# Optimization experiments

Hardware: AMD Instinct MI355X
Metric: run time of the kernel (lower is better)

## Reference

```python
import jax, jax.numpy as jnp
import numpy as np

B, C, H, W = 2, 512, 64, 64
G = 32  # GroupNorm groups
EPS = 1e-6


def setup_inputs() -> dict:
    key = jax.random.key(0)
    ks = jax.random.split(key, 6)
    s = 1.0 / np.sqrt(C)
    return {
        "x": jax.random.normal(ks[0], (B, C, H, W), dtype=jnp.float32),
        "gn_w": jnp.ones((C,), dtype=jnp.float32),
        "gn_b": jnp.zeros((C,), dtype=jnp.float32),
        "wq": jax.random.normal(ks[1], (C, C), dtype=jnp.float32) * s,
        "bq": jnp.zeros((C,), dtype=jnp.float32),
        "wk": jax.random.normal(ks[2], (C, C), dtype=jnp.float32) * s,
        "bk": jnp.zeros((C,), dtype=jnp.float32),
        "wv": jax.random.normal(ks[3], (C, C), dtype=jnp.float32) * s,
        "bv": jnp.zeros((C,), dtype=jnp.float32),
        "wo": jax.random.normal(ks[4], (C, C), dtype=jnp.float32) * s,
        "bo": jnp.zeros((C,), dtype=jnp.float32),
    }


def _group_norm(x, w, b):
    b_, c_, h_, w_ = x.shape
    xg = x.reshape(b_, G, c_ // G, h_ * w_)
    mu = jnp.mean(xg, axis=(2, 3), keepdims=True)
    var = jnp.var(xg, axis=(2, 3), keepdims=True)
    xn = (xg - mu) * jax.lax.rsqrt(var + EPS)
    xn = xn.reshape(b_, c_, h_ * w_)
    return xn * w[None, :, None] + b[None, :, None]  # [B, C, N]


def reference(x, gn_w, gn_b, wq, bq, wk, bk, wv, bv, wo, bo):
    b, c, h, w = x.shape
    hn = _group_norm(x, gn_w, gn_b)  # [B, C, N]
    # 1x1 convs == per-pixel matmuls over channel dim
    q = jnp.einsum('oc,bcn->bon', wq, hn) + bq[None, :, None]
    k = jnp.einsum('oc,bcn->bon', wk, hn) + bk[None, :, None]
    v = jnp.einsum('oc,bcn->bon', wv, hn) + bv[None, :, None]
    scale = jnp.asarray(c, x.dtype) ** -0.5
    attn = jnp.einsum('bci,bcj->bij', q, k) * scale  # [B, N, N]
    attn = jax.nn.softmax(attn, axis=-1)
    o = jnp.einsum('bij,bcj->bci', attn, v)  # [B, C, N]
    o = jnp.einsum('oc,bcn->bon', wo, o) + bo[None, :, None]
    return x + o.reshape(b, c, h, w)
```

## Files before the change

kernel.cpp:

```cpp
#include <hip/hip_runtime.h>

#define CC 512
#define NPIX 4096
#define NB 2
#define NG 32
#define GSIZE 16
#define EPS 1e-6f

typedef unsigned short u16;
typedef __bf16 bf16x8 __attribute__((ext_vector_type(8)));
typedef float f32x4 __attribute__((ext_vector_type(4)));

__device__ __forceinline__ float bf2f(u16 u) {
  union { unsigned int i; float f; } c; c.i = ((unsigned int)u) << 16; return c.f;
}
__device__ __forceinline__ u16 f2bf(float f) {
  union { float f; unsigned int i; } c; c.f = f;
  unsigned int u = c.i;
  return (u16)((u + 0x7fffu + ((u >> 16) & 1u)) >> 16);
}

__global__ __launch_bounds__(256) void f2bf4x4_kernel(
    const float* __restrict__ s0, const float* __restrict__ s1,
    const float* __restrict__ s2, const float* __restrict__ s3,
    u16* __restrict__ d0, u16* __restrict__ d1,
    u16* __restrict__ d2, u16* __restrict__ d3) {
  const float* s; u16* d;
  switch (blockIdx.y) {
    case 0: s = s0; d = d0; break;
    case 1: s = s1; d = d1; break;
    case 2: s = s2; d = d2; break;
    default: s = s3; d = d3; break;
  }
  int i = blockIdx.x * 256 + threadIdx.x;
  float4 v = ((const float4*)s)[i];
  uint2 pk;
  pk.x = (unsigned)f2bf(v.x) | ((unsigned)f2bf(v.y) << 16);
  pk.y = (unsigned)f2bf(v.z) | ((unsigned)f2bf(v.w) << 16);
  ((uint2*)d)[i] = pk;
}

__global__ __launch_bounds__(256) void concat2_kernel(const float* __restrict__ a,
                                                      const float* __restrict__ b,
                                                      float* __restrict__ o) {
  int i = blockIdx.x * 256 + threadIdx.x;
  o[i] = (i < CC) ? a[i] : b[i - CC];
}

__global__ __launch_bounds__(256) void gn_stats_kernel(const float* __restrict__ x,
                                                       float* __restrict__ stats) {
  int bg = blockIdx.x;
  const float4* p = (const float4*)(x + (long)bg * (GSIZE * NPIX));
  float s = 0.f, ss = 0.f;
  for (int i = threadIdx.x; i < GSIZE * NPIX / 4; i += 256) {
    float4 v = p[i];
    s  += v.x + v.y + v.z + v.w;
    ss += v.x * v.x + v.y * v.y + v.z * v.z + v.w * v.w;
  }
  for (int off = 32; off; off >>= 1) { s += __shfl_xor(s, off); ss += __shfl_xor(ss, off); }
  __shared__ float rs[4], rss[4];
  int wid = threadIdx.x >> 6;
  if ((threadIdx.x & 63) == 0) { rs[wid] = s; rss[wid] = ss; }
  __syncthreads();
  if (threadIdx.x == 0) {
    s = rs[0] + rs[1] + rs[2] + rs[3];
    ss = rss[0] + rss[1] + rss[2] + rss[3];
    float mean = s / (float)(GSIZE * NPIX);
    float var = ss / (float)(GSIZE * NPIX) - mean * mean;
    stats[bg * 2] = mean;
    stats[bg * 2 + 1] = rsqrtf(var + EPS);
  }
}

__global__ __launch_bounds__(256) void gn_apply_kernel(const float* __restrict__ x,
                                                       const float* __restrict__ stats,
                                                       const float* __restrict__ gw,
                                                       const float* __restrict__ gb,
                                                       u16* __restrict__ hn) {
  int n0 = blockIdx.x * 64, c0 = blockIdx.y * 64, b = blockIdx.z;
  __shared__ float tile[64][65];
  int t = threadIdx.x;
  int nj = t & 63, cw = t >> 6;
  #pragma unroll
  for (int r = 0; r < 16; ++r) {
    int ci = cw * 16 + r;
    int c = c0 + ci;
    float mean = stats[(b * NG + (c >> 4)) * 2];
    float rstd = stats[(b * NG + (c >> 4)) * 2 + 1];
    float v = x[((long)b * CC + c) * NPIX + n0 + nj];
    tile[ci][nj] = (v - mean) * rstd * gw[c] + gb[c];
  }
  __syncthreads();
  #pragma unroll
  for (int r = 0; r < 16; ++r) {
    int nn = cw * 16 + r;
    hn[((long)b * NPIX + n0 + nn) * CC + c0 + nj] = f2bf(tile[nj][nn]);
  }
}

#define BM 128
#define BN 128
#define BKT 64
#define BUFSZ 8192

template<int OUTF32, int BIASMODE, int RESID>
__global__ __launch_bounds__(256) void gemm_nt(
    const u16* __restrict__ A, int lda, long aBatch,
    const u16* __restrict__ B, int ldb, long bBatch,
    void* __restrict__ C, int ldc, long cBatch,
    const float* __restrict__ bias,
    const float* __restrict__ resid, long rBatch,
    int K, float scale) {
  __shared__ u16 SH[2 * 2 * BUFSZ];
  const int t = threadIdx.x;

  int nwgx = gridDim.x, nwgy = gridDim.y;
  int flat = blockIdx.x + nwgx * (blockIdx.y + nwgy * blockIdx.z);
  int nwg = nwgx * nwgy * gridDim.z;
  int newflat = (flat % 8) * (nwg / 8) + flat / 8;
  const int bx = newflat % nwgx;
  int tmpf = newflat / nwgx;
  const int by = tmpf % nwgy;
  const int bz = tmpf / nwgy;

  const int m0 = by * BM;
  const int n0 = bx * BN;
  const u16* Ab = A + (long)bz * aBatch;
  const u16* Bb = B + (long)bz * bBatch;

  const int lane = t & 63;
  const int wid = t >> 6;
  const int wr = (wid >> 1) * 64;
  const int wc = (wid & 1) * 64;
  const int r16 = lane & 15;
  const int q = lane >> 4;

  const int sRow = wid * 8 + (lane >> 3);
  const int sCol = (((lane & 7) ^ (lane >> 3)) * 8);

  f32x4 acc[4][4] = {};
  const int rsw = r16 & 7;

  const int nt = K / BKT;

  auto stage = [&](int c, int k0) {
    u16* aDst = SH + c * 2 * BUFSZ + wid * 512;
    u16* bDst = SH + c * 2 * BUFSZ + BUFSZ + wid * 512;
    #pragma unroll
    for (int p = 0; p < 4; ++p) {
      __builtin_amdgcn_global_load_lds(
          (const __attribute__((address_space(1))) unsigned int*)(Ab + (long)(m0 + p * 32 + sRow) * lda + k0 + sCol),
          (__attribute__((address_space(3))) unsigned int*)(aDst + p * 2048),
          16, 0, 0);
      __builtin_amdgcn_global_load_lds(
          (const __attribute__((address_space(1))) unsigned int*)(Bb + (long)(n0 + p * 32 + sRow) * ldb + k0 + sCol),
          (__attribute__((address_space(3))) unsigned int*)(bDst + p * 2048),
          16, 0, 0);
    }
  };

  stage(0, 0);

  for (int tt = 0; tt < nt; ++tt) {
    const int pre = tt + 1;
    if (pre < nt) {
      stage(pre & 1, pre * BKT);
      asm volatile("s_waitcnt vmcnt(8)" ::: "memory");
    } else {
      asm volatile("s_waitcnt vmcnt(0)" ::: "memory");
    }
    __builtin_amdgcn_s_barrier();
    __builtin_amdgcn_sched_barrier(0);

    const u16* As_b = SH + (tt & 1) * 2 * BUFSZ;
    const u16* Bs_b = As_b + BUFSZ;
    #pragma unroll
    for (int kk = 0; kk < BKT; kk += 32) {
      bf16x8 af[4], bfr[4];
      const int c0q = (kk >> 3) + q;
      const int colSw = (c0q ^ rsw) * 8;
      #pragma unroll
      for (int i = 0; i < 4; ++i) {
        af[i]  = *(const bf16x8*)&As_b[(wr + i * 16 + r16) * BKT + colSw];
        bfr[i] = *(const bf16x8*)&Bs_b[(wc + i * 16 + r16) * BKT + colSw];
      }
      #pragma unroll
      for (int i = 0; i < 4; ++i)
        #pragma unroll
        for (int j = 0; j < 4; ++j)
          acc[i][j] = __builtin_amdgcn_mfma_f32_16x16x32_bf16(af[i], bfr[j], acc[i][j], 0, 0, 0);
    }
    __builtin_amdgcn_s_barrier();
    __builtin_amdgcn_sched_barrier(0);
  }

  #pragma unroll
  for (int i = 0; i < 4; ++i) {
    #pragma unroll
    for (int j = 0; j < 4; ++j) {
      #pragma unroll
      for (int r = 0; r < 4; ++r) {
        int row = m0 + wr + i * 16 + q * 4 + r;
        int col = n0 + wc + j * 16 + r16;
        float v = acc[i][j][r] * scale;
        if (BIASMODE == 1) v += bias[row];
        if (BIASMODE == 2) v += bias[col];
        long off = (long)bz * cBatch + (long)row * ldc + col;
        if (RESID) v += resid[(long)bz * rBatch + (long)row * ldc + col];
        if (OUTF32) ((float*)C)[off] = v;
        else        ((u16*)C)[off] = f2bf(v);
      }
    }
  }
}

__global__ __launch_bounds__(256) void softmax_kernel(u16* __restrict__ SP, long bStride) {
  u16* p = SP + (long)blockIdx.y * bStride + (long)blockIdx.x * NPIX;
  int t = threadIdx.x;
  float v[16];
  uint4 raw0 = *(const uint4*)(p + t * 8);
  uint4 raw1 = *(const uint4*)(p + 2048 + t * 8);
  const u16* u0 = (const u16*)&raw0;
  const u16* u1 = (const u16*)&raw1;
  #pragma unroll
  for (int i = 0; i < 8; ++i) { v[i] = bf2f(u0[i]); v[8 + i] = bf2f(u1[i]); }
  float m = v[0];
  #pragma unroll
  for (int i = 1; i < 16; ++i) m = fmaxf(m, v[i]);
  for (int off = 32; off; off >>= 1) m = fmaxf(m, __shfl_xor(m, off));
  __shared__ float red[4], red2[4];
  int wid = t >> 6;
  if ((t & 63) == 0) red[wid] = m;
  __syncthreads();
  m = fmaxf(fmaxf(red[0], red[1]), fmaxf(red[2], red[3]));
  float s = 0.f;
  #pragma unroll
  for (int i = 0; i < 16; ++i) { v[i] = __expf(v[i] - m); s += v[i]; }
  for (int off = 32; off; off >>= 1) s += __shfl_xor(s, off);
  if ((t & 63) == 0) red2[wid] = s;
  __syncthreads();
  s = red2[0] + red2[1] + red2[2] + red2[3];
  float inv = 1.0f / s;
  u16 o0[8], o1[8];
  #pragma unroll
  for (int i = 0; i < 8; ++i) { o0[i] = f2bf(v[i] * inv); o1[i] = f2bf(v[8 + i] * inv); }
  *(uint4*)(p + t * 8) = *(uint4*)o0;
  *(uint4*)(p + 2048 + t * 8) = *(uint4*)o1;
}

extern "C" void kernel_launch(void* const* d_in, const int* in_sizes, int n_in,
                              void* d_out, int out_size, void* d_ws, size_t ws_size,
                              hipStream_t stream) {
  const float* x   = (const float*)d_in[0];
  const float* gnw = (const float*)d_in[1];
  const float* gnb = (const float*)d_in[2];
  const float* wq  = (const float*)d_in[3];
  const float* bq  = (const float*)d_in[4];
  const float* wk  = (const float*)d_in[5];
  const float* bk_ = (const float*)d_in[6];
  const float* wv  = (const float*)d_in[7];
  const float* bv  = (const float*)d_in[8];
  const float* wo  = (const float*)d_in[9];
  const float* bo  = (const float*)d_in[10];
  float* out = (float*)d_out;

  char* wsp = (char*)d_ws;
  auto alloc = [&](size_t bytes) {
    char* r = wsp; wsp += (bytes + 255) & ~(size_t)255; return r;
  };
  u16* wqb = (u16*)alloc((size_t)CC * CC * 2);
  u16* wkb = (u16*)alloc((size_t)CC * CC * 2);
  u16* wvb = (u16*)alloc((size_t)CC * CC * 2);
  u16* wob = (u16*)alloc((size_t)CC * CC * 2);
  float* bqk = (float*)alloc((size_t)2 * CC * 4);
  float* stats = (float*)alloc((size_t)NB * NG * 2 * 4);
  u16* hn  = (u16*)alloc((size_t)NB * NPIX * CC * 2);
  u16* qkt = (u16*)alloc((size_t)NB * NPIX * (2 * CC) * 2);
  u16* vcn = (u16*)alloc((size_t)NB * CC * NPIX * 2);
  u16* ot  = (u16*)alloc((size_t)NB * NPIX * CC * 2);
  size_t used = (size_t)(wsp - (char*)d_ws);
  size_t rem = ws_size > used ? ws_size - used : 0;
  int CH = 256;
  if ((size_t)NB * 1024 * NPIX * 2 <= rem) CH = 1024;
  if ((size_t)NB * 4096 * NPIX * 2 <= rem) CH = 4096;
  u16* SP = (u16*)alloc((size_t)NB * CH * NPIX * 2);

  dim3 blk(256);
  f2bf4x4_kernel<<<dim3(CC * CC / 1024, 4), blk, 0, stream>>>(
      wq, wk, wv, wo, wqb, wkb, wvb, wob);
  concat2_kernel<<<2 * CC / 256, blk, 0, stream>>>(bq, bk_, bqk);

  gn_stats_kernel<<<NB * NG, blk, 0, stream>>>(x, stats);
  gn_apply_kernel<<<dim3(NPIX / 64, CC / 64, NB), blk, 0, stream>>>(x, stats, gnw, gnb, hn);

  gemm_nt<0, 2, 0><<<dim3(2 * CC / BN, NPIX / BM, NB), blk, 0, stream>>>(
      hn, CC, (long)NPIX * CC, wqb, CC, 0, qkt, 2 * CC, (long)NPIX * 2 * CC,
      bqk, nullptr, 0, CC, 1.0f);
  gemm_nt<0, 1, 0><<<dim3(NPIX / BN, CC / BM, NB), blk, 0, stream>>>(
      wvb, CC, 0, hn, CC, (long)NPIX * CC, vcn, NPIX, (long)CC * NPIX, bv, nullptr, 0, CC, 1.0f);

  const u16* qt = qkt;
  const u16* kt = qkt + CC;
  const float scale = 0.044194173824159216f;
  for (int i0 = 0; i0 < NPIX; i0 += CH) {
    gemm_nt<0, 0, 0><<<dim3(NPIX / BN, CH / BM, NB), blk, 0, stream>>>(
        qt + (long)i0 * 2 * CC, 2 * CC, (long)NPIX * 2 * CC, kt, 2 * CC, (long)NPIX * 2 * CC,
        SP, NPIX, (long)CH * NPIX, nullptr, nullptr, 0, CC, scale);
    softmax_kernel<<<dim3(CH, NB), blk, 0, stream>>>(SP, (long)CH * NPIX);
    gemm_nt<0, 0, 0><<<dim3(CC / BN, CH / BM, NB), blk, 0, stream>>>(
        SP, NPIX, (long)CH * NPIX, vcn, NPIX, (long)CC * NPIX,
        ot + (long)i0 * CC, CC, (long)NPIX * CC, nullptr, nullptr, 0, NPIX, 1.0f);
  }

  gemm_nt<1, 1, 1><<<dim3(NPIX / BN, CC / BM, NB), blk, 0, stream>>>(
      wob, CC, 0, ot, CC, (long)NPIX * CC, out, NPIX, (long)CC * NPIX,
      bo, x, (long)CC * NPIX, CC, 1.0f);
}
```

Baseline: 188.9 us.

## Add 256x256-tile double-buffered MFMA GEMM for the QK^T score computation

Adds a new 512-thread GEMM kernel with 256x256 output tiles, direct global-to-LDS loads with XOR swizzling, double-buffered K staging, workgroup remapping across XCDs, and setprio around MFMA bursts. It replaces the generic tiled GEMM for the attention score matrix, but only when the whole query range is processed in one chunk (CH == 4096). The aim is more data reuse per tile and overlap of loads with MFMA compute on the largest GEMM. In exchange it uses 128 KB of LDS per block and a large accumulator register footprint, and it is inactive if CH is smaller.

```diff
diff --git a/kernel.cpp b/kernel.cpp
--- a/kernel.cpp
+++ b/kernel.cpp
@@ -212,6 +212,153 @@
       }
     }
   }
+}
+
+__global__ __launch_bounds__(512, 2) void gemm256_nt(
+    const u16* __restrict__ A, int lda, long aBatch,
+    const u16* __restrict__ B, int ldb, long bBatch,
+    u16* __restrict__ C, int ldc, long cBatch,
+    int K, float scale) {
+  __shared__ u16 SH[2][32768];
+  const int t = threadIdx.x;
+
+  int nwgx = gridDim.x, nwgy = gridDim.y;
+  int flat = blockIdx.x + nwgx * (blockIdx.y + nwgy * blockIdx.z);
+  int nwg = nwgx * nwgy * gridDim.z;
+  int newflat = (flat % 8) * (nwg / 8) + flat / 8;
+  const int bx = newflat % nwgx;
+  int tmpf = newflat / nwgx;
+  const int by = tmpf % nwgy;
+  const int bz = tmpf / nwgy;
+
+  const int m0 = by * 256;
+  const int n0 = bx * 256;
+  const u16* Ab = A + (long)bz * aBatch;
+  const u16* Bb = B + (long)bz * bBatch;
+  u16* Cb = C + (long)bz * cBatch;
+
+  const int lane = t & 63;
+  const int wid = t >> 6;
+  const int wrow = (wid >> 2) * 128;
+  const int wcol = (wid & 3) * 64;
+  const int r16 = lane & 15;
+  const int q = lane >> 4;
+  const int rsw = r16 & 7;
+
+  const int sRow = t >> 3;
+  const int sCol = ((t & 7) ^ ((t >> 3) & 7)) * 8;
+
+  auto stage = [&](int d, int k0) {
+    u16* base = &SH[d][0];
+    #pragma unroll
+    for (int i = 0; i < 4; ++i)
+      __builtin_amdgcn_global_load_lds(
+          (const __attribute__((address_space(1))) unsigned int*)(Ab + (long)(m0 + i * 64 + sRow) * lda + k0 + sCol),
+          (__attribute__((address_space(3))) unsigned int*)(base + i * 4096 + wid * 512),
+          16, 0, 0);
+    #pragma unroll
+    for (int i = 0; i < 4; ++i)
+      __builtin_amdgcn_global_load_lds(
+          (const __attribute__((address_space(1))) unsigned int*)(Bb + (long)(n0 + i * 64 + sRow) * ldb + k0 + sCol),
+          (__attribute__((address_space(3))) unsigned int*)(base + 16384 + i * 4096 + wid * 512),
+          16, 0, 0);
+  };
+
+  f32x4 acc[8][4] = {};
+  const int nt = K / 64;
+
+  stage(0, 0);
+
+  for (int tt = 0; tt < nt; ++tt) {
+    const u16* As_ = &SH[tt & 1][0];
+    const u16* Bs_ = As_ + 16384;
+    if (tt + 1 < nt) {
+      stage((tt + 1) & 1, (tt + 1) * 64);
+      asm volatile("s_waitcnt vmcnt(8)" ::: "memory");
+    } else {
+      asm volatile("s_waitcnt vmcnt(0)" ::: "memory");
+    }
+    __builtin_amdgcn_s_barrier();
+    __builtin_amdgcn_sched_barrier(0);
+
+    bf16x8 a0[4], a1[4], b0[4], b1[4];
+    const int c0 = (q ^ rsw) * 8;
+    const int c1 = ((4 + q) ^ rsw) * 8;
+
+    #pragma unroll
+    for (int i = 0; i < 4; ++i)
+      a0[i] = *(const bf16x8*)&As_[(wrow + i * 16 + r16) * 64 + c0];
+    #pragma unroll
+    for (int i = 0; i < 4; ++i)
+      b0[i] = *(const bf16x8*)&Bs_[(wcol + i * 16 + r16) * 64 + c0];
+    asm volatile("s_waitcnt lgkmcnt(0)" ::: "memory");
+    __builtin_amdgcn_sched_barrier(0);
+    __builtin_amdgcn_s_setprio(1);
+    #pragma unroll
+    for (int mi = 0; mi < 4; ++mi)
+      #pragma unroll
+      for (int ni = 0; ni < 4; ++ni)
+        acc[mi][ni] = __builtin_amdgcn_mfma_f32_16x16x32_bf16(a0[mi], b0[ni], acc[mi][ni], 0, 0, 0);
+    __builtin_amdgcn_s_setprio(0);
+    __builtin_amdgcn_s_barrier();
+
+    #pragma unroll
+    for (int i = 0; i < 4; ++i)
+      a1[i] = *(const bf16x8*)&As_[(wrow + (4 + i) * 16 + r16) * 64 + c0];
+    asm volatile("s_waitcnt lgkmcnt(0)" ::: "memory");
+    __builtin_amdgcn_sched_barrier(0);
+    __builtin_amdgcn_s_setprio(1);
+    #pragma unroll
+    for (int mi = 0; mi < 4; ++mi)
+      #pragma unroll
+      for (int ni = 0; ni < 4; ++ni)
+        acc[4 + mi][ni] = __builtin_amdgcn_mfma_f32_16x16x32_bf16(a1[mi], b0[ni], acc[4 + mi][ni], 0, 0, 0);
+    __builtin_amdgcn_s_setprio(0);
+    __builtin_amdgcn_s_barrier();
+
+    #pragma unroll
+    for (int i = 0; i < 4; ++i)
+      a0[i] = *(const bf16x8*)&As_[(wrow + i * 16 + r16) * 64 + c1];
+    #pragma unroll
+    for (int i = 0; i < 4; ++i)
+      b1[i] = *(const bf16x8*)&Bs_[(wcol + i * 16 + r16) * 64 + c1];
+    asm volatile("s_waitcnt lgkmcnt(0)" ::: "memory");
+    __builtin_amdgcn_sched_barrier(0);
+    __builtin_amdgcn_s_setprio(1);
+    #pragma unroll
+    for (int mi = 0; mi < 4; ++mi)
+      #pragma unroll
+      for (int ni = 0; ni < 4; ++ni)
+        acc[mi][ni] = __builtin_amdgcn_mfma_f32_16x16x32_bf16(a0[mi], b1[ni], acc[mi][ni], 0, 0, 0);
+    __builtin_amdgcn_s_setprio(0);
+    __builtin_amdgcn_s_barrier();
+
+    #pragma unroll
+    for (int i = 0; i < 4; ++i)
+      a1[i] = *(const bf16x8*)&As_[(wrow + (4 + i) * 16 + r16) * 64 + c1];
+    asm volatile("s_waitcnt lgkmcnt(0)" ::: "memory");
+    __builtin_amdgcn_sched_barrier(0);
+    __builtin_amdgcn_s_setprio(1);
+    #pragma unroll
+    for (int mi = 0; mi < 4; ++mi)
+      #pragma unroll
+      for (int ni = 0; ni < 4; ++ni)
+        acc[4 + mi][ni] = __builtin_amdgcn_mfma_f32_16x16x32_bf16(a1[mi], b1[ni], acc[4 + mi][ni], 0, 0, 0);
+    __builtin_amdgcn_s_setprio(0);
+    __builtin_amdgcn_s_barrier();
+    __builtin_amdgcn_sched_barrier(0);
+  }
+
+  #pragma unroll
+  for (int mi = 0; mi < 8; ++mi)
+    #pragma unroll
+    for (int ni = 0; ni < 4; ++ni)
+      #pragma unroll
+      for (int r = 0; r < 4; ++r) {
+        int row = m0 + wrow + mi * 16 + q * 4 + r;
+        int col = n0 + wcol + ni * 16 + r16;
+        Cb[(long)row * ldc + col] = f2bf(acc[mi][ni][r] * scale);
+      }
 }
 
 __global__ __launch_bounds__(256) void softmax_kernel(u16* __restrict__ SP, long bStride) {
@@ -303,9 +450,15 @@
   const u16* kt = qkt + CC;
   const float scale = 0.044194173824159216f;
   for (int i0 = 0; i0 < NPIX; i0 += CH) {
-    gemm_nt<0, 0, 0><<<dim3(NPIX / BN, CH / BM, NB), blk, 0, stream>>>(
-        qt + (long)i0 * 2 * CC, 2 * CC, (long)NPIX * 2 * CC, kt, 2 * CC, (long)NPIX * 2 * CC,
-        SP, NPIX, (long)CH * NPIX, nullptr, nullptr, 0, CC, scale);
+    if (CH == 4096) {
+      gemm256_nt<<<dim3(NPIX / 256, NPIX / 256, NB), dim3(512), 0, stream>>>(
+          qt, 2 * CC, (long)NPIX * 2 * CC, kt, 2 * CC, (long)NPIX * 2 * CC,
+          SP, NPIX, (long)CH * NPIX, CC, scale);
+    } else {
+      gemm_nt<0, 0, 0><<<dim3(NPIX / BN, CH / BM, NB), blk, 0, stream>>>(
+          qt + (long)i0 * 2 * CC, 2 * CC, (long)NPIX * 2 * CC, kt, 2 * CC, (long)NPIX * 2 * CC,
+          SP, NPIX, (long)CH * NPIX, nullptr, nullptr, 0, CC, scale);
+    }
     softmax_kernel<<<dim3(CH, NB), blk, 0, stream>>>(SP, (long)CH * NPIX);
     gemm_nt<0, 0, 0><<<dim3(CC / BN, CH / BM, NB), blk, 0, stream>>>(
         SP, NPIX, (long)CH * NPIX, vcn, NPIX, (long)CC * NPIX,
```

New measurement: 179.0 us. -5.2%, faster.
